# Kernel optimization log

Measured on AMD Instinct MI355X. Metric: run time of the kernel, lower is better.

The kernel has to match this reference:

```python
import jax, jax.numpy as jnp
import numpy as np

N_VAR = 50000
N_CON = 50000
N_NODES = N_VAR + N_CON
N_EDGES = 800000
DIM = 64


def _mlp2(x, w1, b1, w2, b2):
    return jnp.maximum(x @ w1 + b1, 0.0) @ w2 + b2


def _edge_conv(x, edge_index, edge_types, w1, b1, w2, b2, num_nodes):
    # PyG MessagePassing flow 'source_to_target': x_j = x[src]=x[edge_index[0]],
    # x_i = x[dst]=x[edge_index[1]]; aggregate mean at dst.
    src, dst = edge_index[0], edge_index[1]
    feats = jnp.concatenate([x[dst], x[src], edge_types], axis=1)  # [E, 2*dim+2]
    msg = _mlp2(feats, w1, b1, w2, b2)                             # [E, dim]
    s = jax.ops.segment_sum(msg, dst, num_segments=num_nodes)
    cnt = jax.ops.segment_sum(jnp.ones((dst.shape[0], 1), msg.dtype), dst,
                              num_segments=num_nodes)
    return s / jnp.maximum(cnt, 1.0)


def setup_inputs() -> dict:
    key = jax.random.key(0)
    ks = jax.random.split(key, 32)

    def w(k, shape, fan_in):
        return jax.random.normal(k, shape, dtype=jnp.float32) * (1.0 / np.sqrt(fan_in))

    inp = {}
    inp['var_node_features'] = jax.random.normal(ks[0], (N_VAR, 2), dtype=jnp.float32)
    inp['con_node_features'] = jax.random.normal(ks[1], (N_CON, 2), dtype=jnp.float32)
    src = jax.random.randint(ks[2], (N_EDGES,), 0, N_NODES)
    dst = jax.random.randint(ks[3], (N_EDGES,), 0, N_NODES)
    inp['edge_index'] = jnp.stack([src, dst]).astype(jnp.int32)
    inp['edge_types'] = jax.random.normal(ks[4], (N_EDGES, 2), dtype=jnp.float32)
    inp['assoc_var'] = jnp.arange(N_VAR, dtype=jnp.int32)
    inp['assoc_con'] = jnp.arange(N_CON, dtype=jnp.int32) + N_VAR
    inp['num_nodes'] = N_NODES

    ki = 5
    for pre in ['var', 'con']:
        inp[f'{pre}_w1'] = w(ks[ki], (2, DIM), 2); ki += 1
        inp[f'{pre}_b1'] = jnp.zeros((DIM,), jnp.float32)
        inp[f'{pre}_w2'] = w(ks[ki], (DIM, DIM), DIM); ki += 1
        inp[f'{pre}_b2'] = jnp.zeros((DIM,), jnp.float32)
    for c in ['conv1', 'conv2', 'conv3']:
        inp[f'{c}_w1'] = w(ks[ki], (2 * DIM + 2, DIM), 2 * DIM + 2); ki += 1
        inp[f'{c}_b1'] = jnp.zeros((DIM,), jnp.float32)
        inp[f'{c}_w2'] = w(ks[ki], (DIM, DIM), DIM); ki += 1
        inp[f'{c}_b2'] = jnp.zeros((DIM,), jnp.float32)
    inp['fc1_w'] = w(ks[ki], (4 * DIM, DIM), 4 * DIM); ki += 1
    inp['fc1_b'] = jnp.zeros((DIM,), jnp.float32)
    inp['fc2_w'] = w(ks[ki], (DIM, DIM), DIM); ki += 1
    inp['fc2_b'] = jnp.zeros((DIM,), jnp.float32)
    inp['fc3_w'] = w(ks[ki], (DIM, 1), DIM); ki += 1
    inp['fc3_b'] = jnp.zeros((1,), jnp.float32)
    return inp


def reference(var_node_features, con_node_features, edge_types,
              var_w1, var_b1, var_w2, var_b2,
              con_w1, con_b1, con_w2, con_b2,
              conv1_w1, conv1_b1, conv1_w2, conv1_b2,
              conv2_w1, conv2_b1, conv2_w2, conv2_b2,
              conv3_w1, conv3_b1, conv3_w2, conv3_b2,
              fc1_w, fc1_b, fc2_w, fc2_b, fc3_w, fc3_b,
              edge_index, assoc_var, assoc_con, num_nodes):
    n = _mlp2(var_node_features, var_w1, var_b1, var_w2, var_b2)  # [n_var, dim]
    e = _mlp2(con_node_features, con_w1, con_b1, con_w2, con_b2)  # [n_con, dim]
    x = jnp.zeros((num_nodes, n.shape[-1]), dtype=n.dtype)
    x = x.at[assoc_var].set(n)
    x = x.at[assoc_con].set(e)
    xs = [x]
    xs.append(jnp.maximum(_edge_conv(xs[-1], edge_index, edge_types,
                                     conv1_w1, conv1_b1, conv1_w2, conv1_b2, num_nodes), 0.0))
    xs.append(jnp.maximum(_edge_conv(xs[-1], edge_index, edge_types,
                                     conv2_w1, conv2_b1, conv2_w2, conv2_b2, num_nodes), 0.0))
    xs.append(jnp.maximum(_edge_conv(xs[-1], edge_index, edge_types,
                                     conv3_w1, conv3_b1, conv3_w2, conv3_b2, num_nodes), 0.0))
    h = jnp.concatenate(xs, axis=-1)[assoc_var]          # [n_var, 4*dim]
    h = jnp.maximum(h @ fc1_w + fc1_b, 0.0)
    h = jnp.maximum(h @ fc2_w + fc2_b, 0.0)
    out = jax.nn.sigmoid(h @ fc3_w + fc3_b)
    return out.squeeze(-1)
```

## Files before the change

kernel.cpp:

```cpp
#include <hip/hip_runtime.h>
#include <hip/hip_bf16.h>
#include <math.h>


#define N_VARN 50000
#define NNODES 100000
#define NEDGES 800000
#define NB_SCAN 196

typedef __hip_bfloat16 bf16;

__device__ __forceinline__ float b2f(unsigned short u) {
  union { unsigned v; float f; } x;
  x.v = ((unsigned)u) << 16;
  return x.f;
}

__global__ __launch_bounds__(256) void embed_kernel(
    const float* __restrict__ vf, const float* __restrict__ cf,
    const float* __restrict__ vw1, const float* __restrict__ vb1,
    const float* __restrict__ vw2, const float* __restrict__ vb2,
    const float* __restrict__ cw1, const float* __restrict__ cb1,
    const float* __restrict__ cw2, const float* __restrict__ cb2,
    const int* __restrict__ av, const int* __restrict__ ac,
    bf16* __restrict__ x0) {
  __shared__ float sh[40][64];
  int tid = threadIdx.x, wid = tid >> 6, lane = tid & 63;
  int nodebase = blockIdx.x * 40;
  bool con = (nodebase >= N_VARN);
  const float* in = con ? cf : vf;
  const float* w1 = con ? cw1 : vw1;
  const float* b1 = con ? cb1 : vb1;
  const float* w2 = con ? cw2 : vw2;
  const float* b2 = con ? cb2 : vb2;
  const int* assoc = con ? ac : av;
  int ibase = con ? (nodebase - N_VARN) : nodebase;
  float w1a = w1[lane], w1b = w1[64 + lane], b1v = b1[lane];
  int n0 = wid * 10;
#pragma unroll 1
  for (int j = 0; j < 10; ++j) {
    int ni = ibase + n0 + j;
    float i0 = in[ni * 2], i1 = in[ni * 2 + 1];
    sh[n0 + j][lane] = fmaxf(fmaf(i0, w1a, fmaf(i1, w1b, b1v)), 0.f);
  }
  float acc[10];
  float b2v = b2[lane];
#pragma unroll
  for (int j = 0; j < 10; ++j) acc[j] = b2v;
#pragma unroll 2
  for (int k4 = 0; k4 < 16; ++k4) {
    float w0 = w2[(k4 * 4 + 0) * 64 + lane];
    float w1v = w2[(k4 * 4 + 1) * 64 + lane];
    float w2v = w2[(k4 * 4 + 2) * 64 + lane];
    float w3v = w2[(k4 * 4 + 3) * 64 + lane];
#pragma unroll
    for (int j = 0; j < 10; ++j) {
      float4 hv = *(const float4*)&sh[n0 + j][k4 * 4];
      acc[j] = fmaf(hv.x, w0, acc[j]);
      acc[j] = fmaf(hv.y, w1v, acc[j]);
      acc[j] = fmaf(hv.z, w2v, acc[j]);
      acc[j] = fmaf(hv.w, w3v, acc[j]);
    }
  }
#pragma unroll
  for (int j = 0; j < 10; ++j) {
    int row = assoc[ibase + n0 + j];
    x0[(size_t)row * 64 + lane] = __float2bfloat16(acc[j]);
  }
}

__global__ __launch_bounds__(256) void hist_kernel(const int* __restrict__ ei,
                                                   unsigned* __restrict__ deg) {
  int e = blockIdx.x * 256 + threadIdx.x;
  atomicAdd(&deg[ei[NEDGES + e]], 1u);
}

__global__ __launch_bounds__(512) void scan1_kernel(
    const unsigned* __restrict__ deg, unsigned* __restrict__ blocksum) {
  __shared__ unsigned sm[512];
  int t = threadIdx.x;
  int i = blockIdx.x * 512 + t;
  sm[t] = (i < NNODES) ? deg[i] : 0u;
  __syncthreads();
  for (int off = 256; off > 0; off >>= 1) {
    if (t < off) sm[t] += sm[t + off];
    __syncthreads();
  }
  if (t == 0) blocksum[blockIdx.x] = sm[0];
}

__global__ __launch_bounds__(256) void scan2_kernel(
    const unsigned* __restrict__ blocksum, unsigned* __restrict__ blockoff) {
  __shared__ unsigned sm[256];
  int t = threadIdx.x;
  sm[t] = (t < NB_SCAN) ? blocksum[t] : 0u;
  __syncthreads();
  if (t == 0) {
    unsigned run = 0;
    for (int j = 0; j < NB_SCAN; ++j) {
      unsigned v = sm[j];
      sm[j] = run;
      run += v;
    }
  }
  __syncthreads();
  if (t < NB_SCAN) blockoff[t] = sm[t];
}

__global__ __launch_bounds__(512) void scan3_kernel(
    const unsigned* __restrict__ deg, const unsigned* __restrict__ blockoff,
    unsigned* __restrict__ rowptr) {
  __shared__ unsigned sm[512];
  int t = threadIdx.x;
  int i = blockIdx.x * 512 + t;
  unsigned v = (i < NNODES) ? deg[i] : 0u;
  sm[t] = v;
  __syncthreads();
  for (int off = 1; off < 512; off <<= 1) {
    unsigned add = (t >= off) ? sm[t - off] : 0u;
    __syncthreads();
    sm[t] += add;
    __syncthreads();
  }
  if (i <= NNODES) rowptr[i] = blockoff[blockIdx.x] + sm[t] - v;
}

__global__ __launch_bounds__(256) void scatter_kernel(
    const int* __restrict__ ei, const float* __restrict__ et,
    const unsigned* __restrict__ rowptr, unsigned* __restrict__ cursor,
    int* __restrict__ colsrc, float2* __restrict__ colet) {
  int e = blockIdx.x * 256 + threadIdx.x;
  int d = ei[NEDGES + e];
  unsigned pos = rowptr[d] + atomicAdd(&cursor[d], 1u);
  colsrc[pos] = ei[e];
  colet[pos] = ((const float2*)et)[e];
}

__global__ __launch_bounds__(256) void proj_kernel(
    const bf16* __restrict__ x, const float* __restrict__ w1,
    const float* __restrict__ b1,
    bf16* __restrict__ A16, bf16* __restrict__ B16) {
  __shared__ float sh[40][64];
  int tid = threadIdx.x, wid = tid >> 6, lane = tid & 63;
  int nodebase = blockIdx.x * 40;
  for (int idx = tid; idx < 40 * 16; idx += 256) {
    int n = idx >> 4, c4 = idx & 15;
    ushort4 u = *(const ushort4*)((const unsigned short*)x +
                                  (size_t)(nodebase + n) * 64 + c4 * 4);
    float4 v = make_float4(b2f(u.x), b2f(u.y), b2f(u.z), b2f(u.w));
    *(float4*)&sh[n][c4 * 4] = v;
  }
  __syncthreads();
  int n0 = wid * 10;
  float aa[10], bb[10];
  float b1v = b1[lane];
#pragma unroll
  for (int j = 0; j < 10; ++j) {
    aa[j] = b1v;
    bb[j] = 0.f;
  }
#pragma unroll 2
  for (int k4 = 0; k4 < 16; ++k4) {
    float wa0 = w1[(k4 * 4 + 0) * 64 + lane];
    float wa1 = w1[(k4 * 4 + 1) * 64 + lane];
    float wa2 = w1[(k4 * 4 + 2) * 64 + lane];
    float wa3 = w1[(k4 * 4 + 3) * 64 + lane];
    float wb0 = w1[(64 + k4 * 4 + 0) * 64 + lane];
    float wb1 = w1[(64 + k4 * 4 + 1) * 64 + lane];
    float wb2 = w1[(64 + k4 * 4 + 2) * 64 + lane];
    float wb3 = w1[(64 + k4 * 4 + 3) * 64 + lane];
#pragma unroll
    for (int j = 0; j < 10; ++j) {
      float4 xv = *(const float4*)&sh[n0 + j][k4 * 4];
      aa[j] = fmaf(xv.x, wa0, aa[j]);
      aa[j] = fmaf(xv.y, wa1, aa[j]);
      aa[j] = fmaf(xv.z, wa2, aa[j]);
      aa[j] = fmaf(xv.w, wa3, aa[j]);
      bb[j] = fmaf(xv.x, wb0, bb[j]);
      bb[j] = fmaf(xv.y, wb1, bb[j]);
      bb[j] = fmaf(xv.z, wb2, bb[j]);
      bb[j] = fmaf(xv.w, wb3, bb[j]);
    }
  }
#pragma unroll
  for (int j = 0; j < 10; ++j) {
    A16[(size_t)(nodebase + n0 + j) * 64 + lane] = __float2bfloat16(aa[j]);
    B16[(size_t)(nodebase + n0 + j) * 64 + lane] = __float2bfloat16(bb[j]);
  }
}

__global__ __launch_bounds__(256) void agg_kernel(
    const unsigned* __restrict__ rowptr, const int* __restrict__ colsrc,
    const float2* __restrict__ colet, const bf16* __restrict__ A16,
    const bf16* __restrict__ B16, const float* __restrict__ w1c,
    const float* __restrict__ w2, const float* __restrict__ b2,
    bf16* __restrict__ xout) {
  __shared__ float sh[40][64];
  __shared__ float shc[40];
  int tid = threadIdx.x, wid = tid >> 6, lane = tid & 63;
  int half = lane >> 5;
  int fl = lane & 31;
  int nodebase = blockIdx.x * 40;
  int n0 = wid * 10;
  float2 c0p = *(const float2*)&w1c[fl * 2];
  float2 c1p = *(const float2*)&w1c[64 + fl * 2];
#pragma unroll 1
  for (int j = 0; j < 10; ++j) {
    int node = nodebase + n0 + j;
    unsigned beg = rowptr[node], end = rowptr[node + 1];
    ushort2 au = *(const ushort2*)((const unsigned short*)A16 +
                                   (size_t)node * 64 + fl * 2);
    float ax = b2f(au.x), ay = b2f(au.y);
    float accx0 = 0.f, accy0 = 0.f, accx1 = 0.f, accy1 = 0.f;
    unsigned i = beg;
    for (; i + 4 <= end; i += 4) {
      int sA = colsrc[i + half];
      int sB = colsrc[i + 2 + half];
      float2 tA = colet[i + half];
      float2 tB = colet[i + 2 + half];
      ushort2 buA = *(const ushort2*)((const unsigned short*)B16 +
                                      (size_t)sA * 64 + fl * 2);
      ushort2 buB = *(const ushort2*)((const unsigned short*)B16 +
                                      (size_t)sB * 64 + fl * 2);
      accx0 += fmaxf(ax + b2f(buA.x) + fmaf(tA.x, c0p.x, tA.y * c1p.x), 0.f);
      accy0 += fmaxf(ay + b2f(buA.y) + fmaf(tA.x, c0p.y, tA.y * c1p.y), 0.f);
      accx1 += fmaxf(ax + b2f(buB.x) + fmaf(tB.x, c0p.x, tB.y * c1p.x), 0.f);
      accy1 += fmaxf(ay + b2f(buB.y) + fmaf(tB.x, c0p.y, tB.y * c1p.y), 0.f);
    }
    for (; i < end; i += 2) {
      if (i + half < end) {
        int s = colsrc[i + half];
        float2 t = colet[i + half];
        ushort2 bu = *(const ushort2*)((const unsigned short*)B16 +
                                       (size_t)s * 64 + fl * 2);
        accx0 += fmaxf(ax + b2f(bu.x) + fmaf(t.x, c0p.x, t.y * c1p.x), 0.f);
        accy0 += fmaxf(ay + b2f(bu.y) + fmaf(t.x, c0p.y, t.y * c1p.y), 0.f);
      }
    }
    float accx = accx0 + accx1;
    float accy = accy0 + accy1;
    accx += __shfl_xor(accx, 32);
    accy += __shfl_xor(accy, 32);
    if (half == 0) *(float2*)&sh[n0 + j][fl * 2] = make_float2(accx, accy);
    if (lane == 0) shc[n0 + j] = (float)(end - beg);
  }
  float o[10];
  float b2l = b2[lane];
#pragma unroll
  for (int j = 0; j < 10; ++j) o[j] = shc[n0 + j] * b2l;
#pragma unroll 2
  for (int k4 = 0; k4 < 16; ++k4) {
    float w0 = w2[(k4 * 4 + 0) * 64 + lane];
    float w1v = w2[(k4 * 4 + 1) * 64 + lane];
    float w2v = w2[(k4 * 4 + 2) * 64 + lane];
    float w3v = w2[(k4 * 4 + 3) * 64 + lane];
#pragma unroll
    for (int j = 0; j < 10; ++j) {
      float4 sv = *(const float4*)&sh[n0 + j][k4 * 4];
      o[j] = fmaf(sv.x, w0, o[j]);
      o[j] = fmaf(sv.y, w1v, o[j]);
      o[j] = fmaf(sv.z, w2v, o[j]);
      o[j] = fmaf(sv.w, w3v, o[j]);
    }
  }
#pragma unroll
  for (int j = 0; j < 10; ++j) {
    float cn = shc[n0 + j];
    float r = o[j] / fmaxf(cn, 1.f);
    xout[(size_t)(nodebase + n0 + j) * 64 + lane] =
        __float2bfloat16(fmaxf(r, 0.f));
  }
}

#define HB_NODES 40
#define HB_NPW 10
__global__ __launch_bounds__(256) void head_kernel(
    const bf16* __restrict__ x0, const bf16* __restrict__ x1,
    const bf16* __restrict__ x2, const bf16* __restrict__ x3,
    const int* __restrict__ av,
    const float* __restrict__ fc1w, const float* __restrict__ fc1b,
    const float* __restrict__ fc2w, const float* __restrict__ fc2b,
    const float* __restrict__ fc3w, const float* __restrict__ fc3b,
    float* __restrict__ out) {
  __shared__ float h[HB_NODES][256];
  int tid = threadIdx.x;
  int nodebase = blockIdx.x * HB_NODES;
  for (int idx = tid; idx < HB_NODES * 16; idx += 256) {
    int n = idx >> 4, c4 = idx & 15;
    int row = av[nodebase + n];
    const unsigned short* p0 = (const unsigned short*)x0 + (size_t)row * 64;
    const unsigned short* p1 = (const unsigned short*)x1 + (size_t)row * 64;
    const unsigned short* p2 = (const unsigned short*)x2 + (size_t)row * 64;
    const unsigned short* p3 = (const unsigned short*)x3 + (size_t)row * 64;
    ushort4 u0 = *(const ushort4*)(p0 + c4 * 4);
    ushort4 u1 = *(const ushort4*)(p1 + c4 * 4);
    ushort4 u2 = *(const ushort4*)(p2 + c4 * 4);
    ushort4 u3 = *(const ushort4*)(p3 + c4 * 4);
    float* dstp = &h[n][0];
    *(float4*)(dstp + c4 * 4) =
        make_float4(b2f(u0.x), b2f(u0.y), b2f(u0.z), b2f(u0.w));
    *(float4*)(dstp + 64 + c4 * 4) =
        make_float4(b2f(u1.x), b2f(u1.y), b2f(u1.z), b2f(u1.w));
    *(float4*)(dstp + 128 + c4 * 4) =
        make_float4(b2f(u2.x), b2f(u2.y), b2f(u2.z), b2f(u2.w));
    *(float4*)(dstp + 192 + c4 * 4) =
        make_float4(b2f(u3.x), b2f(u3.y), b2f(u3.z), b2f(u3.w));
  }
  __syncthreads();
  int wid = tid >> 6, lane = tid & 63;
  int n0 = wid * HB_NPW;
  float acc[HB_NPW];
#pragma unroll
  for (int j = 0; j < HB_NPW; ++j) acc[j] = fc1b[lane];
#pragma unroll 2
  for (int k4 = 0; k4 < 64; ++k4) {
    float w0 = fc1w[(k4 * 4 + 0) * 64 + lane];
    float w1v = fc1w[(k4 * 4 + 1) * 64 + lane];
    float w2v = fc1w[(k4 * 4 + 2) * 64 + lane];
    float w3v = fc1w[(k4 * 4 + 3) * 64 + lane];
#pragma unroll
    for (int j = 0; j < HB_NPW; ++j) {
      float4 hv = *(const float4*)&h[n0 + j][k4 * 4];
      acc[j] = fmaf(hv.x, w0, acc[j]);
      acc[j] = fmaf(hv.y, w1v, acc[j]);
      acc[j] = fmaf(hv.z, w2v, acc[j]);
      acc[j] = fmaf(hv.w, w3v, acc[j]);
    }
  }
  __syncthreads();
  float* h2 = &h[0][0];
#pragma unroll
  for (int j = 0; j < HB_NPW; ++j) h2[(n0 + j) * 64 + lane] = fmaxf(acc[j], 0.f);
  __syncthreads();
  float acc2[HB_NPW];
#pragma unroll
  for (int j = 0; j < HB_NPW; ++j) acc2[j] = fc2b[lane];
#pragma unroll 2
  for (int k4 = 0; k4 < 16; ++k4) {
    float w0 = fc2w[(k4 * 4 + 0) * 64 + lane];
    float w1v = fc2w[(k4 * 4 + 1) * 64 + lane];
    float w2v = fc2w[(k4 * 4 + 2) * 64 + lane];
    float w3v = fc2w[(k4 * 4 + 3) * 64 + lane];
#pragma unroll
    for (int j = 0; j < HB_NPW; ++j) {
      float4 hv = *(const float4*)&h2[(n0 + j) * 64 + k4 * 4];
      acc2[j] = fmaf(hv.x, w0, acc2[j]);
      acc2[j] = fmaf(hv.y, w1v, acc2[j]);
      acc2[j] = fmaf(hv.z, w2v, acc2[j]);
      acc2[j] = fmaf(hv.w, w3v, acc2[j]);
    }
  }
  float w3l = fc3w[lane];
  float b3 = fc3b[0];
#pragma unroll
  for (int j = 0; j < HB_NPW; ++j) {
    float p = fmaxf(acc2[j], 0.f) * w3l;
#pragma unroll
    for (int off = 32; off; off >>= 1) p += __shfl_xor(p, off);
    if (lane == j) out[nodebase + n0 + j] = 1.f / (1.f + expf(-(p + b3)));
  }
}

extern "C" void kernel_launch(void* const* d_in, const int* in_sizes, int n_in,
                              void* d_out, int out_size, void* d_ws,
                              size_t ws_size, hipStream_t stream) {
  const float* vf = (const float*)d_in[0];
  const float* cf = (const float*)d_in[1];
  const int* ei = (const int*)d_in[2];
  const float* et = (const float*)d_in[3];
  const int* av = (const int*)d_in[4];
  const int* ac = (const int*)d_in[5];
  const float* vw1 = (const float*)d_in[7];
  const float* vb1 = (const float*)d_in[8];
  const float* vw2 = (const float*)d_in[9];
  const float* vb2 = (const float*)d_in[10];
  const float* cw1 = (const float*)d_in[11];
  const float* cb1 = (const float*)d_in[12];
  const float* cw2 = (const float*)d_in[13];
  const float* cb2 = (const float*)d_in[14];
  const float* convw1[3] = {(const float*)d_in[15], (const float*)d_in[19],
                            (const float*)d_in[23]};
  const float* convb1[3] = {(const float*)d_in[16], (const float*)d_in[20],
                            (const float*)d_in[24]};
  const float* convw2[3] = {(const float*)d_in[17], (const float*)d_in[21],
                            (const float*)d_in[25]};
  const float* convb2[3] = {(const float*)d_in[18], (const float*)d_in[22],
                            (const float*)d_in[26]};
  const float* fc1w = (const float*)d_in[27];
  const float* fc1b = (const float*)d_in[28];
  const float* fc2w = (const float*)d_in[29];
  const float* fc2b = (const float*)d_in[30];
  const float* fc3w = (const float*)d_in[31];
  const float* fc3b = (const float*)d_in[32];

  char* wsb = (char*)d_ws;
  const size_t ROWB16 = (size_t)NNODES * 64 * sizeof(bf16);
  bf16* x[4];
  x[0] = (bf16*)(wsb);
  x[1] = (bf16*)(wsb + ROWB16);
  x[2] = (bf16*)(wsb + 2 * ROWB16);
  x[3] = (bf16*)(wsb + 3 * ROWB16);
  bf16* A16 = (bf16*)(wsb + 4 * ROWB16);
  bf16* B16 = (bf16*)(wsb + 5 * ROWB16);
  float2* colet = (float2*)(wsb + 6 * ROWB16);
  int* colsrc = (int*)((char*)colet + NEDGES * 8);
  unsigned* rowptr = (unsigned*)(colsrc + NEDGES);
  unsigned* deg = rowptr + NNODES + 1;
  unsigned* cursor = deg + NNODES;
  unsigned* blocksum = cursor + NNODES;
  unsigned* blockoff = blocksum + 256;

  embed_kernel<<<NNODES / 40, 256, 0, stream>>>(vf, cf, vw1, vb1, vw2, vb2,
                                                cw1, cb1, cw2, cb2, av, ac,
                                                x[0]);

  hipMemsetAsync(deg, 0, 2 * NNODES * sizeof(unsigned), stream);
  hist_kernel<<<NEDGES / 256, 256, 0, stream>>>(ei, deg);
  scan1_kernel<<<NB_SCAN, 512, 0, stream>>>(deg, blocksum);
  scan2_kernel<<<1, 256, 0, stream>>>(blocksum, blockoff);
  scan3_kernel<<<NB_SCAN, 512, 0, stream>>>(deg, blockoff, rowptr);
  scatter_kernel<<<NEDGES / 256, 256, 0, stream>>>(ei, et, rowptr, cursor,
                                                   colsrc, colet);

  for (int c = 0; c < 3; ++c) {
    proj_kernel<<<NNODES / 40, 256, 0, stream>>>(x[c], convw1[c], convb1[c],
                                                 A16, B16);
    int agg_blocks = (c == 2) ? (N_VARN / 40) : (NNODES / 40);
    agg_kernel<<<agg_blocks, 256, 0, stream>>>(
        rowptr, colsrc, colet, A16, B16, convw1[c] + 128 * 64, convw2[c],
        convb2[c], x[c + 1]);
  }

  head_kernel<<<N_VARN / HB_NODES, 256, 0, stream>>>(
      x[0], x[1], x[2], x[3], av, fc1w, fc1b, fc2w, fc2b, fc3w, fc3b,
      (float*)d_out);
}
```

Measured before the change: 638.6 us.

## Fuse node projection into embed and aggregation kernels, pack edge records

Removes the separate proj_kernel launches by computing the next layer's A/B projections inside the embed kernel and at the end of each aggregation kernel, with ping-pong A/B buffers. Edge source and type are packed into a single 16-byte record so each edge needs one load instead of two. The head kernel moves to 512 threads with 5 nodes per wave. This saves three launches and the re-read of x, at the cost of more registers in the aggregation kernel and 4 wasted bytes of padding per edge.

New measurement: 578.6 us. -9.4%, faster.

```diff
diff --git a/kernel.cpp b/kernel.cpp
--- a/kernel.cpp
+++ b/kernel.cpp
@@ -23,7 +23,8 @@
     const float* __restrict__ cw1, const float* __restrict__ cb1,
     const float* __restrict__ cw2, const float* __restrict__ cb2,
     const int* __restrict__ av, const int* __restrict__ ac,
-    bf16* __restrict__ x0) {
+    const float* __restrict__ nw1, const float* __restrict__ nb1,
+    bf16* __restrict__ x0, bf16* __restrict__ A16, bf16* __restrict__ B16) {
   __shared__ float sh[40][64];
   int tid = threadIdx.x, wid = tid >> 6, lane = tid & 63;
   int nodebase = blockIdx.x * 40;
@@ -37,9 +38,11 @@
   int ibase = con ? (nodebase - N_VARN) : nodebase;
   float w1a = w1[lane], w1b = w1[64 + lane], b1v = b1[lane];
   int n0 = wid * 10;
+  int rows[10];
 #pragma unroll 1
   for (int j = 0; j < 10; ++j) {
     int ni = ibase + n0 + j;
+    rows[j] = assoc[ni];
     float i0 = in[ni * 2], i1 = in[ni * 2 + 1];
     sh[n0 + j][lane] = fmaxf(fmaf(i0, w1a, fmaf(i1, w1b, b1v)), 0.f);
   }
@@ -64,111 +67,26 @@
   }
 #pragma unroll
   for (int j = 0; j < 10; ++j) {
-    int row = assoc[ibase + n0 + j];
-    x0[(size_t)row * 64 + lane] = __float2bfloat16(acc[j]);
-  }
-}
-
-__global__ __launch_bounds__(256) void hist_kernel(const int* __restrict__ ei,
-                                                   unsigned* __restrict__ deg) {
-  int e = blockIdx.x * 256 + threadIdx.x;
-  atomicAdd(&deg[ei[NEDGES + e]], 1u);
-}
-
-__global__ __launch_bounds__(512) void scan1_kernel(
-    const unsigned* __restrict__ deg, unsigned* __restrict__ blocksum) {
-  __shared__ unsigned sm[512];
-  int t = threadIdx.x;
-  int i = blockIdx.x * 512 + t;
-  sm[t] = (i < NNODES) ? deg[i] : 0u;
-  __syncthreads();
-  for (int off = 256; off > 0; off >>= 1) {
-    if (t < off) sm[t] += sm[t + off];
-    __syncthreads();
-  }
-  if (t == 0) blocksum[blockIdx.x] = sm[0];
-}
-
-__global__ __launch_bounds__(256) void scan2_kernel(
-    const unsigned* __restrict__ blocksum, unsigned* __restrict__ blockoff) {
-  __shared__ unsigned sm[256];
-  int t = threadIdx.x;
-  sm[t] = (t < NB_SCAN) ? blocksum[t] : 0u;
-  __syncthreads();
-  if (t == 0) {
-    unsigned run = 0;
-    for (int j = 0; j < NB_SCAN; ++j) {
-      unsigned v = sm[j];
-      sm[j] = run;
-      run += v;
-    }
-  }
-  __syncthreads();
-  if (t < NB_SCAN) blockoff[t] = sm[t];
-}
-
-__global__ __launch_bounds__(512) void scan3_kernel(
-    const unsigned* __restrict__ deg, const unsigned* __restrict__ blockoff,
-    unsigned* __restrict__ rowptr) {
-  __shared__ unsigned sm[512];
-  int t = threadIdx.x;
-  int i = blockIdx.x * 512 + t;
-  unsigned v = (i < NNODES) ? deg[i] : 0u;
-  sm[t] = v;
-  __syncthreads();
-  for (int off = 1; off < 512; off <<= 1) {
-    unsigned add = (t >= off) ? sm[t - off] : 0u;
-    __syncthreads();
-    sm[t] += add;
-    __syncthreads();
-  }
-  if (i <= NNODES) rowptr[i] = blockoff[blockIdx.x] + sm[t] - v;
-}
-
-__global__ __launch_bounds__(256) void scatter_kernel(
-    const int* __restrict__ ei, const float* __restrict__ et,
-    const unsigned* __restrict__ rowptr, unsigned* __restrict__ cursor,
-    int* __restrict__ colsrc, float2* __restrict__ colet) {
-  int e = blockIdx.x * 256 + threadIdx.x;
-  int d = ei[NEDGES + e];
-  unsigned pos = rowptr[d] + atomicAdd(&cursor[d], 1u);
-  colsrc[pos] = ei[e];
-  colet[pos] = ((const float2*)et)[e];
-}
-
-__global__ __launch_bounds__(256) void proj_kernel(
-    const bf16* __restrict__ x, const float* __restrict__ w1,
-    const float* __restrict__ b1,
-    bf16* __restrict__ A16, bf16* __restrict__ B16) {
-  __shared__ float sh[40][64];
-  int tid = threadIdx.x, wid = tid >> 6, lane = tid & 63;
-  int nodebase = blockIdx.x * 40;
-  for (int idx = tid; idx < 40 * 16; idx += 256) {
-    int n = idx >> 4, c4 = idx & 15;
-    ushort4 u = *(const ushort4*)((const unsigned short*)x +
-                                  (size_t)(nodebase + n) * 64 + c4 * 4);
-    float4 v = make_float4(b2f(u.x), b2f(u.y), b2f(u.z), b2f(u.w));
-    *(float4*)&sh[n][c4 * 4] = v;
-  }
-  __syncthreads();
-  int n0 = wid * 10;
+    x0[(size_t)rows[j] * 64 + lane] = __float2bfloat16(acc[j]);
+    sh[n0 + j][lane] = acc[j];
+  }
   float aa[10], bb[10];
-  float b1v = b1[lane];
-#pragma unroll
-  for (int j = 0; j < 10; ++j) {
-    aa[j] = b1v;
+  float nb1v = nb1[lane];
+#pragma unroll
+  for (int j = 0; j < 10; ++j) {
+    aa[j] = nb1v;
     bb[j] = 0.f;
   }
 #pragma unroll 2
   for (int k4 = 0; k4 < 16; ++k4) {
-    float wa0 = w1[(k4 * 4 + 0) * 64 + lane];
-    float wa1 = w1[(k4 * 4 + 1) * 64 + lane];
-    float wa2 = w1[(k4 * 4 + 2) * 64 + lane];
-    float wa3 = w1[(k4 * 4 + 3) * 64 + lane];
-    float wb0 = w1[(64 + k4 * 4 + 0) * 64 + lane];
-    float wb1 = w1[(64 + k4 * 4 + 1) * 64 + lane];
-    float wb2 = w1[(64 + k4 * 4 + 2) * 64 + lane];
-    float wb3 = w1[(64 + k4 * 4 + 3) * 64 + lane];
+    float wa0 = nw1[(k4 * 4 + 0) * 64 + lane];
+    float wa1 = nw1[(k4 * 4 + 1) * 64 + lane];
+    float wa2 = nw1[(k4 * 4 + 2) * 64 + lane];
+    float wa3 = nw1[(k4 * 4 + 3) * 64 + lane];
+    float wb0 = nw1[(64 + k4 * 4 + 0) * 64 + lane];
+    float wb1 = nw1[(64 + k4 * 4 + 1) * 64 + lane];
+    float wb2 = nw1[(64 + k4 * 4 + 2) * 64 + lane];
+    float wb3 = nw1[(64 + k4 * 4 + 3) * 64 + lane];
 #pragma unroll
     for (int j = 0; j < 10; ++j) {
       float4 xv = *(const float4*)&sh[n0 + j][k4 * 4];
@@ -184,17 +102,91 @@
   }
 #pragma unroll
   for (int j = 0; j < 10; ++j) {
-    A16[(size_t)(nodebase + n0 + j) * 64 + lane] = __float2bfloat16(aa[j]);
-    B16[(size_t)(nodebase + n0 + j) * 64 + lane] = __float2bfloat16(bb[j]);
-  }
-}
-
+    A16[(size_t)rows[j] * 64 + lane] = __float2bfloat16(aa[j]);
+    B16[(size_t)rows[j] * 64 + lane] = __float2bfloat16(bb[j]);
+  }
+}
+
+__global__ __launch_bounds__(256) void hist_kernel(const int* __restrict__ ei,
+                                                   unsigned* __restrict__ deg) {
+  int e = blockIdx.x * 256 + threadIdx.x;
+  atomicAdd(&deg[ei[NEDGES + e]], 1u);
+}
+
+__global__ __launch_bounds__(512) void scan1_kernel(
+    const unsigned* __restrict__ deg, unsigned* __restrict__ blocksum) {
+  __shared__ unsigned sm[512];
+  int t = threadIdx.x;
+  int i = blockIdx.x * 512 + t;
+  sm[t] = (i < NNODES) ? deg[i] : 0u;
+  __syncthreads();
+  for (int off = 256; off > 0; off >>= 1) {
+    if (t < off) sm[t] += sm[t + off];
+    __syncthreads();
+  }
+  if (t == 0) blocksum[blockIdx.x] = sm[0];
+}
+
+__global__ __launch_bounds__(256) void scan2_kernel(
+    const unsigned* __restrict__ blocksum, unsigned* __restrict__ blockoff) {
+  __shared__ unsigned sm[256];
+  int t = threadIdx.x;
+  sm[t] = (t < NB_SCAN) ? blocksum[t] : 0u;
+  __syncthreads();
+  if (t == 0) {
+    unsigned run = 0;
+    for (int j = 0; j < NB_SCAN; ++j) {
+      unsigned v = sm[j];
+      sm[j] = run;
+      run += v;
+    }
+  }
+  __syncthreads();
+  if (t < NB_SCAN) blockoff[t] = sm[t];
+}
+
+__global__ __launch_bounds__(512) void scan3_kernel(
+    const unsigned* __restrict__ deg, const unsigned* __restrict__ blockoff,
+    unsigned* __restrict__ rowptr) {
+  __shared__ unsigned sm[512];
+  int t = threadIdx.x;
+  int i = blockIdx.x * 512 + t;
+  unsigned v = (i < NNODES) ? deg[i] : 0u;
+  sm[t] = v;
+  __syncthreads();
+  for (int off = 1; off < 512; off <<= 1) {
+    unsigned add = (t >= off) ? sm[t - off] : 0u;
+    __syncthreads();
+    sm[t] += add;
+    __syncthreads();
+  }
+  if (i <= NNODES) rowptr[i] = blockoff[blockIdx.x] + sm[t] - v;
+}
+
+__global__ __launch_bounds__(256) void scatter_kernel(
+    const int* __restrict__ ei, const float* __restrict__ et,
+    const unsigned* __restrict__ rowptr, unsigned* __restrict__ cursor,
+    int4* __restrict__ erec) {
+  int e = blockIdx.x * 256 + threadIdx.x;
+  int d = ei[NEDGES + e];
+  float2 t = ((const float2*)et)[e];
+  unsigned pos = rowptr[d] + atomicAdd(&cursor[d], 1u);
+  int4 r;
+  r.x = ei[e];
+  r.y = __float_as_int(t.x);
+  r.z = __float_as_int(t.y);
+  r.w = 0;
+  erec[pos] = r;
+}
+
+template <bool FUSE>
 __global__ __launch_bounds__(256) void agg_kernel(
-    const unsigned* __restrict__ rowptr, const int* __restrict__ colsrc,
-    const float2* __restrict__ colet, const bf16* __restrict__ A16,
-    const bf16* __restrict__ B16, const float* __restrict__ w1c,
-    const float* __restrict__ w2, const float* __restrict__ b2,
-    bf16* __restrict__ xout) {
+    const unsigned* __restrict__ rowptr, const int4* __restrict__ erec,
+    const bf16* __restrict__ A16i, const bf16* __restrict__ B16i,
+    const float* __restrict__ w1c, const float* __restrict__ w2,
+    const float* __restrict__ b2, bf16* __restrict__ xout,
+    const float* __restrict__ nw1, const float* __restrict__ nb1,
+    bf16* __restrict__ A16o, bf16* __restrict__ B16o) {
   __shared__ float sh[40][64];
   __shared__ float shc[40];
   int tid = threadIdx.x, wid = tid >> 6, lane = tid & 63;
@@ -208,33 +200,33 @@
   for (int j = 0; j < 10; ++j) {
     int node = nodebase + n0 + j;
     unsigned beg = rowptr[node], end = rowptr[node + 1];
-    ushort2 au = *(const ushort2*)((const unsigned short*)A16 +
+    ushort2 au = *(const ushort2*)((const unsigned short*)A16i +
                                    (size_t)node * 64 + fl * 2);
     float ax = b2f(au.x), ay = b2f(au.y);
     float accx0 = 0.f, accy0 = 0.f, accx1 = 0.f, accy1 = 0.f;
     unsigned i = beg;
     for (; i + 4 <= end; i += 4) {
-      int sA = colsrc[i + half];
-      int sB = colsrc[i + 2 + half];
-      float2 tA = colet[i + half];
-      float2 tB = colet[i + 2 + half];
-      ushort2 buA = *(const ushort2*)((const unsigned short*)B16 +
-                                      (size_t)sA * 64 + fl * 2);
-      ushort2 buB = *(const ushort2*)((const unsigned short*)B16 +
-                                      (size_t)sB * 64 + fl * 2);
-      accx0 += fmaxf(ax + b2f(buA.x) + fmaf(tA.x, c0p.x, tA.y * c1p.x), 0.f);
-      accy0 += fmaxf(ay + b2f(buA.y) + fmaf(tA.x, c0p.y, tA.y * c1p.y), 0.f);
-      accx1 += fmaxf(ax + b2f(buB.x) + fmaf(tB.x, c0p.x, tB.y * c1p.x), 0.f);
-      accy1 += fmaxf(ay + b2f(buB.y) + fmaf(tB.x, c0p.y, tB.y * c1p.y), 0.f);
+      int4 rA = erec[i + half];
+      int4 rB = erec[i + 2 + half];
+      float tAx = __int_as_float(rA.y), tAy = __int_as_float(rA.z);
+      float tBx = __int_as_float(rB.y), tBy = __int_as_float(rB.z);
+      ushort2 buA = *(const ushort2*)((const unsigned short*)B16i +
+                                      (size_t)rA.x * 64 + fl * 2);
+      ushort2 buB = *(const ushort2*)((const unsigned short*)B16i +
+                                      (size_t)rB.x * 64 + fl * 2);
+      accx0 += fmaxf(ax + b2f(buA.x) + fmaf(tAx, c0p.x, tAy * c1p.x), 0.f);
+      accy0 += fmaxf(ay + b2f(buA.y) + fmaf(tAx, c0p.y, tAy * c1p.y), 0.f);
+      accx1 += fmaxf(ax + b2f(buB.x) + fmaf(tBx, c0p.x, tBy * c1p.x), 0.f);
+      accy1 += fmaxf(ay + b2f(buB.y) + fmaf(tBx, c0p.y, tBy * c1p.y), 0.f);
     }
     for (; i < end; i += 2) {
       if (i + half < end) {
-        int s = colsrc[i + half];
-        float2 t = colet[i + half];
-        ushort2 bu = *(const ushort2*)((const unsigned short*)B16 +
-                                       (size_t)s * 64 + fl * 2);
-        accx0 += fmaxf(ax + b2f(bu.x) + fmaf(t.x, c0p.x, t.y * c1p.x), 0.f);
-        accy0 += fmaxf(ay + b2f(bu.y) + fmaf(t.x, c0p.y, t.y * c1p.y), 0.f);
+        int4 r = erec[i + half];
+        float tx = __int_as_float(r.y), ty = __int_as_float(r.z);
+        ushort2 bu = *(const ushort2*)((const unsigned short*)B16i +
+                                       (size_t)r.x * 64 + fl * 2);
+        accx0 += fmaxf(ax + b2f(bu.x) + fmaf(tx, c0p.x, ty * c1p.x), 0.f);
+        accy0 += fmaxf(ay + b2f(bu.y) + fmaf(tx, c0p.y, ty * c1p.y), 0.f);
       }
     }
     float accx = accx0 + accx1;
@@ -266,15 +258,54 @@
 #pragma unroll
   for (int j = 0; j < 10; ++j) {
     float cn = shc[n0 + j];
-    float r = o[j] / fmaxf(cn, 1.f);
-    xout[(size_t)(nodebase + n0 + j) * 64 + lane] =
-        __float2bfloat16(fmaxf(r, 0.f));
+    float r = fmaxf(o[j] / fmaxf(cn, 1.f), 0.f);
+    o[j] = r;
+    xout[(size_t)(nodebase + n0 + j) * 64 + lane] = __float2bfloat16(r);
+  }
+  if (FUSE) {
+#pragma unroll
+    for (int j = 0; j < 10; ++j) sh[n0 + j][lane] = o[j];
+    float aa[10], bb[10];
+    float nb1v = nb1[lane];
+#pragma unroll
+    for (int j = 0; j < 10; ++j) {
+      aa[j] = nb1v;
+      bb[j] = 0.f;
+    }
+#pragma unroll 2
+    for (int k4 = 0; k4 < 16; ++k4) {
+      float wa0 = nw1[(k4 * 4 + 0) * 64 + lane];
+      float wa1 = nw1[(k4 * 4 + 1) * 64 + lane];
+      float wa2 = nw1[(k4 * 4 + 2) * 64 + lane];
+      float wa3 = nw1[(k4 * 4 + 3) * 64 + lane];
+      float wb0 = nw1[(64 + k4 * 4 + 0) * 64 + lane];
+      float wb1 = nw1[(64 + k4 * 4 + 1) * 64 + lane];
+      float wb2 = nw1[(64 + k4 * 4 + 2) * 64 + lane];
+      float wb3 = nw1[(64 + k4 * 4 + 3) * 64 + lane];
+#pragma unroll
+      for (int j = 0; j < 10; ++j) {
+        float4 xv = *(const float4*)&sh[n0 + j][k4 * 4];
+        aa[j] = fmaf(xv.x, wa0, aa[j]);
+        aa[j] = fmaf(xv.y, wa1, aa[j]);
+        aa[j] = fmaf(xv.z, wa2, aa[j]);
+        aa[j] = fmaf(xv.w, wa3, aa[j]);
+        bb[j] = fmaf(xv.x, wb0, bb[j]);
+        bb[j] = fmaf(xv.y, wb1, bb[j]);
+        bb[j] = fmaf(xv.z, wb2, bb[j]);
+        bb[j] = fmaf(xv.w, wb3, bb[j]);
+      }
+    }
+#pragma unroll
+    for (int j = 0; j < 10; ++j) {
+      A16o[(size_t)(nodebase + n0 + j) * 64 + lane] = __float2bfloat16(aa[j]);
+      B16o[(size_t)(nodebase + n0 + j) * 64 + lane] = __float2bfloat16(bb[j]);
+    }
   }
 }
 
 #define HB_NODES 40
-#define HB_NPW 10
-__global__ __launch_bounds__(256) void head_kernel(
+#define HB_NPW 5
+__global__ __launch_bounds__(512) void head_kernel(
     const bf16* __restrict__ x0, const bf16* __restrict__ x1,
     const bf16* __restrict__ x2, const bf16* __restrict__ x3,
     const int* __restrict__ av,
@@ -285,7 +316,7 @@
   __shared__ float h[HB_NODES][256];
   int tid = threadIdx.x;
   int nodebase = blockIdx.x * HB_NODES;
-  for (int idx = tid; idx < HB_NODES * 16; idx += 256) {
+  for (int idx = tid; idx < HB_NODES * 16; idx += 512) {
     int n = idx >> 4, c4 = idx & 15;
     int row = av[nodebase + n];
     const unsigned short* p0 = (const unsigned short*)x0 + (size_t)row * 64;
@@ -402,17 +433,18 @@
   x[3] = (bf16*)(wsb + 3 * ROWB16);
   bf16* A16 = (bf16*)(wsb + 4 * ROWB16);
   bf16* B16 = (bf16*)(wsb + 5 * ROWB16);
-  float2* colet = (float2*)(wsb + 6 * ROWB16);
-  int* colsrc = (int*)((char*)colet + NEDGES * 8);
-  unsigned* rowptr = (unsigned*)(colsrc + NEDGES);
+  bf16* A16b = (bf16*)(wsb + 6 * ROWB16);
+  bf16* B16b = (bf16*)(wsb + 7 * ROWB16);
+  int4* erec = (int4*)(wsb + 8 * ROWB16);
+  unsigned* rowptr = (unsigned*)((char*)erec + (size_t)NEDGES * 16);
   unsigned* deg = rowptr + NNODES + 1;
   unsigned* cursor = deg + NNODES;
   unsigned* blocksum = cursor + NNODES;
   unsigned* blockoff = blocksum + 256;
 
-  embed_kernel<<<NNODES / 40, 256, 0, stream>>>(vf, cf, vw1, vb1, vw2, vb2,
-                                                cw1, cb1, cw2, cb2, av, ac,
-                                                x[0]);
+  embed_kernel<<<NNODES / 40, 256, 0, stream>>>(
+      vf, cf, vw1, vb1, vw2, vb2, cw1, cb1, cw2, cb2, av, ac, convw1[0],
+      convb1[0], x[0], A16, B16);
 
   hipMemsetAsync(deg, 0, 2 * NNODES * sizeof(unsigned), stream);
   hist_kernel<<<NEDGES / 256, 256, 0, stream>>>(ei, deg);
@@ -420,18 +452,19 @@
   scan2_kernel<<<1, 256, 0, stream>>>(blocksum, blockoff);
   scan3_kernel<<<NB_SCAN, 512, 0, stream>>>(deg, blockoff, rowptr);
   scatter_kernel<<<NEDGES / 256, 256, 0, stream>>>(ei, et, rowptr, cursor,
-                                                   colsrc, colet);
-
-  for (int c = 0; c < 3; ++c) {
-    proj_kernel<<<NNODES / 40, 256, 0, stream>>>(x[c], convw1[c], convb1[c],
-                                                 A16, B16);
-    int agg_blocks = (c == 2) ? (N_VARN / 40) : (NNODES / 40);
-    agg_kernel<<<agg_blocks, 256, 0, stream>>>(
-        rowptr, colsrc, colet, A16, B16, convw1[c] + 128 * 64, convw2[c],
-        convb2[c], x[c + 1]);
-  }
-
-  head_kernel<<<N_VARN / HB_NODES, 256, 0, stream>>>(
+                                                   erec);
+
+  agg_kernel<true><<<NNODES / 40, 256, 0, stream>>>(
+      rowptr, erec, A16, B16, convw1[0] + 128 * 64, convw2[0], convb2[0],
+      x[1], convw1[1], convb1[1], A16b, B16b);
+  agg_kernel<true><<<NNODES / 40, 256, 0, stream>>>(
+      rowptr, erec, A16b, B16b, convw1[1] + 128 * 64, convw2[1], convb2[1],
+      x[2], convw1[2], convb1[2], A16, B16);
+  agg_kernel<false><<<N_VARN / 40, 256, 0, stream>>>(
+      rowptr, erec, A16, B16, convw1[2] + 128 * 64, convw2[2], convb2[2],
+      x[3], nullptr, nullptr, nullptr, nullptr);
+
+  head_kernel<<<N_VARN / HB_NODES, 512, 0, stream>>>(
       x[0], x[1], x[2], x[3], av, fc1w, fc1b, fc2w, fc2b, fc3w, fc3b,
       (float*)d_out);
 }
```
